# Performance work log

Hardware: AMD Instinct MI355X
Metric: run time of the kernel (lower is better)

## Reference

```python
import jax, jax.numpy as jnp
import numpy as np

EPS = 1e-5  # BatchNorm eps (torch default)


def setup_inputs() -> dict:
    key = jax.random.key(0)
    ks = jax.random.split(key, 12)
    C, Ci, B, H, W = 64, 32, 2, 96, 96  # plane, inter_plane=plane//2

    def n(k, shape, s=0.05):
        return jax.random.normal(k, shape, jnp.float32) * s

    return {
        "xA": jax.random.normal(ks[0], (B, C, H, W), jnp.float32),
        "xB": jax.random.normal(ks[1], (B, C, H, W), jnp.float32),
        "Wk": n(ks[2], (Ci, C)), "bk": n(ks[3], (Ci,)),
        "Wv": n(ks[4], (Ci, C)), "bv": n(ks[5], (Ci,)),
        "Wq": n(ks[6], (Ci, C)), "bq": n(ks[7], (Ci,)),
        "Wg": n(ks[8], (Ci, Ci)),  # conv_wg, 1x1 Conv1d, no bias
        "g1_gamma": jnp.ones((Ci,), jnp.float32), "g1_beta": jnp.zeros((Ci,), jnp.float32),
        "g1_mean": jnp.zeros((Ci,), jnp.float32), "g1_var": jnp.ones((Ci,), jnp.float32),
        "Wo": n(ks[9], (C, Ci)), "bo": n(ks[10], (C,)),
        "g2_gamma": jnp.ones((C,), jnp.float32), "g2_beta": jnp.zeros((C,), jnp.float32),
        "g2_mean": jnp.zeros((C,), jnp.float32), "g2_var": jnp.ones((C,), jnp.float32),
    }


def reference(xA, xB, Wk, bk, Wv, bv, Wq, bq, Wg,
              g1_gamma, g1_beta, g1_mean, g1_var,
              Wo, bo, g2_gamma, g2_beta, g2_mean, g2_var):
    B, C, H, W = xB.shape
    N = H * W
    # 1x1 conv2d projections -> [B, Ci, N]
    k = (jnp.einsum('bchw,oc->bohw', xA, Wk) + bk[None, :, None, None]).reshape(B, -1, N)
    v = (jnp.einsum('bchw,oc->bohw', xA, Wv) + bv[None, :, None, None]).reshape(B, -1, N)
    q = (jnp.einsum('bchw,oc->bohw', xB, Wq) + bq[None, :, None, None]).reshape(B, -1, N)
    # AV = softmax(v^T @ q, axis=2)  -> [B, N, N]
    A = jax.nn.softmax(jnp.einsum('bcn,bcm->bnm', v, q), axis=2)
    # k @ AV -> [B, Ci, N]
    av = jnp.einsum('bcn,bnm->bcm', k, A)
    # conv_wg (1x1 conv1d, no bias) + BatchNorm1d (inference form)
    av = jnp.einsum('oc,bcn->bon', Wg, av)
    av = (av - g1_mean[None, :, None]) * (g1_gamma / jnp.sqrt(g1_var + EPS))[None, :, None] + g1_beta[None, :, None]
    av = av.reshape(B, -1, H, W)
    # out: 1x1 conv2d -> plane, BatchNorm2d, residual, relu
    o = jnp.einsum('oc,bchw->bohw', Wo, av) + bo[None, :, None, None]
    o = (o - g2_mean[None, :, None, None]) * (g2_gamma / jnp.sqrt(g2_var + EPS))[None, :, None, None] + g2_beta[None, :, None, None]
    return jax.nn.relu(o + xB)
```

## Files before the change

kernel.cpp:

```cpp
#include <hip/hip_runtime.h>
#include <hip/hip_bf16.h>

#define CI 32
#define CC 64
#define NBATCH 2
#define NPIX 9216
#define NSD 16
#define LOG2E 1.4426950408889634f

typedef __attribute__((ext_vector_type(8))) short s16x8;
typedef __attribute__((ext_vector_type(4))) short s16x4;
typedef __attribute__((ext_vector_type(4))) float f32x4;
typedef __attribute__((ext_vector_type(2))) unsigned int u32x2;
typedef __attribute__((ext_vector_type(4))) unsigned int u32x4;

static __device__ __forceinline__ unsigned cvtpk(float a, float b) {
    unsigned d;
    asm("v_cvt_pk_bf16_f32 %0, %1, %2" : "=v"(d) : "v"(a), "v"(b));
    return d;
}
static __device__ __forceinline__ short f2b(float f) {
    union { float f; unsigned u; } v; v.f = f;
    return (short)((v.u + 0x7FFFu + ((v.u >> 16) & 1u)) >> 16);
}
static __device__ __forceinline__ float b2f(short s) {
    union { unsigned u; float f; } v; v.u = ((unsigned)(unsigned short)s) << 16;
    return v.f;
}

__global__ __launch_bounds__(256) void k_proj(
    const float* __restrict__ xA, const float* __restrict__ xB,
    const float* __restrict__ Wk, const float* __restrict__ bk,
    const float* __restrict__ Wv, const float* __restrict__ bv,
    const float* __restrict__ Wq, const float* __restrict__ bq,
    short* __restrict__ vT, short* __restrict__ qT, short* __restrict__ kC)
{
    int mode = blockIdx.y;
    const float* W    = mode == 0 ? Wk : (mode == 1 ? Wv : Wq);
    const float* bias = mode == 0 ? bk : (mode == 1 ? bv : bq);
    const float* X    = mode == 2 ? xB : xA;

    __shared__ float sW[CI * CC];
    __shared__ float sb[CI];
    __shared__ float spart[3][64][33];
    for (int i = threadIdx.x; i < CI * CC; i += 256) sW[i] = W[i];
    if (threadIdx.x < CI) sb[threadIdx.x] = bias[threadIdx.x];
    __syncthreads();

    int q4 = threadIdx.x >> 6;
    int lp = threadIdx.x & 63;
    int idx = blockIdx.x * 64 + lp;
    int b = idx / NPIX, n = idx % NPIX;

    float acc[CI];
    #pragma unroll
    for (int o = 0; o < CI; o++) acc[o] = 0.f;

    const float* px = X + (size_t)b * CC * NPIX + n;
    #pragma unroll
    for (int cc = 0; cc < 16; cc++) {
        int c = q4 * 16 + cc;
        float x = px[(size_t)c * NPIX];
        #pragma unroll
        for (int o = 0; o < CI; o++) acc[o] += sW[o * CC + c] * x;
    }
    if (q4) {
        #pragma unroll
        for (int o = 0; o < CI; o++) spart[q4 - 1][lp][o] = acc[o];
    }
    __syncthreads();
    if (q4 == 0) {
        #pragma unroll
        for (int o = 0; o < CI; o++)
            acc[o] += spart[0][lp][o] + spart[1][lp][o] + spart[2][lp][o] + sb[o];
        if (mode == 0) {
            #pragma unroll
            for (int o = 0; o < CI; o++)
                kC[((size_t)b * CI + o) * NPIX + n] = f2b(acc[o]);
        } else {
            float sc = (mode == 2) ? LOG2E : 1.0f;
            short* dst = (mode == 1 ? vT : qT) + ((size_t)b * NPIX + n) * CI;
            #pragma unroll
            for (int v4 = 0; v4 < 4; v4++) {
                u32x4 pk;
                #pragma unroll
                for (int j = 0; j < 4; j++)
                    pk[j] = cvtpk(acc[v4 * 8 + 2 * j] * sc, acc[v4 * 8 + 2 * j + 1] * sc);
                ((u32x4*)dst)[v4] = pk;
            }
        }
    }
}

__global__ __launch_bounds__(128) void k_denom(
    const short* __restrict__ vT, const short* __restrict__ qT,
    float* __restrict__ sum_part)
{
    int w = threadIdx.x >> 6, lane = threadIdx.x & 63;
    int r = lane & 15, g = lane >> 4;
    int b = blockIdx.y;
    int nb = blockIdx.x * 64 + w * 32;

    const short* vb = vT + (size_t)b * NPIX * CI;
    s16x8 a0 = *(const s16x8*)(vb + (size_t)(nb + r) * CI + 8 * g);
    s16x8 a1 = *(const s16x8*)(vb + (size_t)(nb + 16 + r) * CI + 8 * g);

    f32x4 s0 = {0.f, 0.f, 0.f, 0.f}, s1 = {0.f, 0.f, 0.f, 0.f};
    f32x4 z  = {0.f, 0.f, 0.f, 0.f};
    const short* qb = qT + (size_t)b * NPIX * CI;
    int mlo = blockIdx.z * (NPIX / NSD);
    int mhi = mlo + NPIX / NSD;
    for (int m0 = mlo; m0 < mhi; m0 += 32) {
        s16x8 q0 = *(const s16x8*)(qb + (size_t)(m0 + r) * CI + 8 * g);
        s16x8 q1 = *(const s16x8*)(qb + (size_t)(m0 + 16 + r) * CI + 8 * g);
        f32x4 t00 = __builtin_amdgcn_mfma_f32_16x16x32_bf16(a0, q0, z, 0, 0, 0);
        f32x4 t01 = __builtin_amdgcn_mfma_f32_16x16x32_bf16(a0, q1, z, 0, 0, 0);
        f32x4 t10 = __builtin_amdgcn_mfma_f32_16x16x32_bf16(a1, q0, z, 0, 0, 0);
        f32x4 t11 = __builtin_amdgcn_mfma_f32_16x16x32_bf16(a1, q1, z, 0, 0, 0);
        #pragma unroll
        for (int e = 0; e < 4; e++) {
            s0[e] += __builtin_amdgcn_exp2f(t00[e]) + __builtin_amdgcn_exp2f(t01[e]);
            s1[e] += __builtin_amdgcn_exp2f(t10[e]) + __builtin_amdgcn_exp2f(t11[e]);
        }
    }
    #pragma unroll
    for (int mask = 1; mask < 16; mask <<= 1) {
        #pragma unroll
        for (int e = 0; e < 4; e++) {
            s0[e] += __shfl_xor(s0[e], mask, 64);
            s1[e] += __shfl_xor(s1[e], mask, 64);
        }
    }
    if (r == 0) {
        float* sp = sum_part + ((size_t)blockIdx.z * NBATCH + b) * NPIX;
        #pragma unroll
        for (int e = 0; e < 4; e++) {
            sp[nb + 4 * g + e]      = s0[e];
            sp[nb + 16 + 4 * g + e] = s1[e];
        }
    }
}

__global__ __launch_bounds__(256) void k_invd(
    const float* __restrict__ sum_part, float* __restrict__ invd)
{
    int idx = blockIdx.x * 256 + threadIdx.x;
    float s = 0.f;
    #pragma unroll
    for (int zz = 0; zz < NSD; zz++)
        s += sum_part[(size_t)zz * NBATCH * NPIX + idx];
    invd[idx] = 1.0f / s;
}

__global__ __launch_bounds__(256) void k_scale(
    short* __restrict__ kC, const float* __restrict__ invd)
{
    int idx = blockIdx.x * 256 + threadIdx.x;
    int n = idx % NPIX;
    int b = idx / (CI * NPIX);
    kC[idx] = f2b(b2f(kC[idx]) * invd[b * NPIX + n]);
}

__global__ __launch_bounds__(128) void k_attn(
    const short* __restrict__ vT, const short* __restrict__ qT,
    const short* __restrict__ kC, short* __restrict__ avp, int slice)
{
    __shared__ short plds[2][32][36];
    int w = threadIdx.x >> 6, lane = threadIdx.x & 63;
    int r = lane & 15, g = lane >> 4;
    int b = blockIdx.y;
    int m0 = blockIdx.x * 64 + w * 32;

    const short* qb = qT + (size_t)b * NPIX * CI;
    s16x8 qb0 = *(const s16x8*)(qb + (size_t)(m0 + r) * CI + 8 * g);
    s16x8 qb1 = *(const s16x8*)(qb + (size_t)(m0 + 16 + r) * CI + 8 * g);

    const short* vb = vT + (size_t)b * NPIX * CI;
    const short* k0 = kC + ((size_t)b * CI + r) * NPIX;
    const short* k1 = k0 + (size_t)16 * NPIX;

    f32x4 acc00 = {0,0,0,0}, acc01 = {0,0,0,0}, acc10 = {0,0,0,0}, acc11 = {0,0,0,0};
    f32x4 z = {0,0,0,0};

    int nlo = blockIdx.z * slice;
    int nhi = nlo + slice;
    for (int n0 = nlo; n0 < nhi; n0 += 32) {
        s16x8 a0  = *(const s16x8*)(vb + (size_t)(n0 + r) * CI + 8 * g);
        s16x8 a1  = *(const s16x8*)(vb + (size_t)(n0 + 16 + r) * CI + 8 * g);
        s16x8 ka0 = *(const s16x8*)(k0 + n0 + 8 * g);
        s16x8 ka1 = *(const s16x8*)(k1 + n0 + 8 * g);

        f32x4 t00 = __builtin_amdgcn_mfma_f32_16x16x32_bf16(a0, qb0, z, 0, 0, 0);
        f32x4 t01 = __builtin_amdgcn_mfma_f32_16x16x32_bf16(a0, qb1, z, 0, 0, 0);
        f32x4 t10 = __builtin_amdgcn_mfma_f32_16x16x32_bf16(a1, qb0, z, 0, 0, 0);
        f32x4 t11 = __builtin_amdgcn_mfma_f32_16x16x32_bf16(a1, qb1, z, 0, 0, 0);

        u32x2 w00 = {cvtpk(__builtin_amdgcn_exp2f(t00[0]), __builtin_amdgcn_exp2f(t00[1])),
                     cvtpk(__builtin_amdgcn_exp2f(t00[2]), __builtin_amdgcn_exp2f(t00[3]))};
        u32x2 w10 = {cvtpk(__builtin_amdgcn_exp2f(t10[0]), __builtin_amdgcn_exp2f(t10[1])),
                     cvtpk(__builtin_amdgcn_exp2f(t10[2]), __builtin_amdgcn_exp2f(t10[3]))};
        u32x2 w01 = {cvtpk(__builtin_amdgcn_exp2f(t01[0]), __builtin_amdgcn_exp2f(t01[1])),
                     cvtpk(__builtin_amdgcn_exp2f(t01[2]), __builtin_amdgcn_exp2f(t01[3]))};
        u32x2 w11 = {cvtpk(__builtin_amdgcn_exp2f(t11[0]), __builtin_amdgcn_exp2f(t11[1])),
                     cvtpk(__builtin_amdgcn_exp2f(t11[2]), __builtin_amdgcn_exp2f(t11[3]))};

        *(u32x2*)&plds[w][r][4 * g]           = w00;
        *(u32x2*)&plds[w][r][16 + 4 * g]      = w10;
        *(u32x2*)&plds[w][16 + r][4 * g]      = w01;
        *(u32x2*)&plds[w][16 + r][16 + 4 * g] = w11;

        s16x4 l0 = *(const s16x4*)&plds[w][r][8 * g];
        s16x4 h0 = *(const s16x4*)&plds[w][r][8 * g + 4];
        s16x4 l1 = *(const s16x4*)&plds[w][16 + r][8 * g];
        s16x4 h1 = *(const s16x4*)&plds[w][16 + r][8 * g + 4];
        s16x8 pb0 = {l0[0], l0[1], l0[2], l0[3], h0[0], h0[1], h0[2], h0[3]};
        s16x8 pb1 = {l1[0], l1[1], l1[2], l1[3], h1[0], h1[1], h1[2], h1[3]};

        acc00 = __builtin_amdgcn_mfma_f32_16x16x32_bf16(ka0, pb0, acc00, 0, 0, 0);
        acc10 = __builtin_amdgcn_mfma_f32_16x16x32_bf16(ka1, pb0, acc10, 0, 0, 0);
        acc01 = __builtin_amdgcn_mfma_f32_16x16x32_bf16(ka0, pb1, acc01, 0, 0, 0);
        acc11 = __builtin_amdgcn_mfma_f32_16x16x32_bf16(ka1, pb1, acc11, 0, 0, 0);
    }

    short* dst = avp + ((size_t)blockIdx.z * NBATCH + b) * NPIX * CI;
    u32x2 o00 = {cvtpk(acc00[0], acc00[1]), cvtpk(acc00[2], acc00[3])};
    u32x2 o10 = {cvtpk(acc10[0], acc10[1]), cvtpk(acc10[2], acc10[3])};
    u32x2 o01 = {cvtpk(acc01[0], acc01[1]), cvtpk(acc01[2], acc01[3])};
    u32x2 o11 = {cvtpk(acc11[0], acc11[1]), cvtpk(acc11[2], acc11[3])};
    *(u32x2*)(dst + (size_t)(m0 + r) * CI + 4 * g)           = o00;
    *(u32x2*)(dst + (size_t)(m0 + r) * CI + 16 + 4 * g)      = o10;
    *(u32x2*)(dst + (size_t)(m0 + 16 + r) * CI + 4 * g)      = o01;
    *(u32x2*)(dst + (size_t)(m0 + 16 + r) * CI + 16 + 4 * g) = o11;
}

__global__ __launch_bounds__(256) void e_red(
    const short* __restrict__ avp, short* __restrict__ av, int nsa)
{
    int vecidx = blockIdx.x * 256 + threadIdx.x;
    const short* src = avp + (size_t)vecidx * 8;
    float s[8];
    #pragma unroll
    for (int j = 0; j < 8; j++) s[j] = 0.f;
    for (int zz = 0; zz < nsa; zz++) {
        s16x8 t = *(const s16x8*)(src + (size_t)zz * NBATCH * NPIX * CI);
        #pragma unroll
        for (int j = 0; j < 8; j++) s[j] += b2f(t[j]);
    }
    u32x4 pk;
    #pragma unroll
    for (int j = 0; j < 4; j++) pk[j] = cvtpk(s[2 * j], s[2 * j + 1]);
    *(u32x4*)(av + (size_t)vecidx * 8) = pk;
}

__global__ __launch_bounds__(256) void e_fused(
    const short* __restrict__ av,
    const float* __restrict__ Wg,
    const float* __restrict__ g1g, const float* __restrict__ g1b,
    const float* __restrict__ g1m, const float* __restrict__ g1v,
    const float* __restrict__ Wo, const float* __restrict__ bo,
    const float* __restrict__ g2g, const float* __restrict__ g2b,
    const float* __restrict__ g2m, const float* __restrict__ g2v,
    const float* __restrict__ xB, float* __restrict__ out)
{
    __shared__ float sWg[CI * CI], sWo[32 * CI], s1[CI], t1[CI], s2[32], t2[32];
    int t = threadIdx.x, jh = blockIdx.y;
    for (int i = t; i < CI * CI; i += 256) sWg[i] = Wg[i];
    for (int i = t; i < 32 * CI; i += 256) sWo[i] = Wo[jh * 32 * CI + i];
    if (t < CI) {
        float s = g1g[t] * rsqrtf(g1v[t] + 1e-5f);
        s1[t] = s; t1[t] = g1b[t] - g1m[t] * s;
    } else if (t < CI + 32) {
        int j = jh * 32 + (t - CI);
        float s = g2g[j] * rsqrtf(g2v[j] + 1e-5f);
        s2[t - CI] = s; t2[t - CI] = g2b[j] - g2m[j] * s + bo[j] * s;
    }
    __syncthreads();

    int idx = blockIdx.x * 256 + t;
    int b = idx / NPIX, m = idx % NPIX;

    float a[CI];
    const short* p = av + (size_t)idx * CI;
    #pragma unroll
    for (int v8 = 0; v8 < 4; v8++) {
        s16x8 tv = *(const s16x8*)(p + 8 * v8);
        #pragma unroll
        for (int j = 0; j < 8; j++) a[8 * v8 + j] = b2f(tv[j]);
    }
    float a2[CI];
    #pragma unroll
    for (int o = 0; o < CI; o++) {
        float acc = 0.f;
        #pragma unroll
        for (int c = 0; c < CI; c++) acc += sWg[o * CI + c] * a[c];
        a2[o] = acc * s1[o] + t1[o];
    }
    #pragma unroll
    for (int jj = 0; jj < 32; jj++) {
        float acc = 0.f;
        #pragma unroll
        for (int o = 0; o < CI; o++) acc += sWo[jj * CI + o] * a2[o];
        acc = acc * s2[jj] + t2[jj];
        size_t oi = ((size_t)b * CC + jh * 32 + jj) * NPIX + m;
        float res = acc + xB[oi];
        out[oi] = res > 0.f ? res : 0.f;
    }
}

extern "C" void kernel_launch(void* const* d_in, const int* in_sizes, int n_in,
                              void* d_out, int out_size, void* d_ws, size_t ws_size,
                              hipStream_t stream)
{
    const float* xA = (const float*)d_in[0];
    const float* xB = (const float*)d_in[1];
    const float* Wk = (const float*)d_in[2];
    const float* bk = (const float*)d_in[3];
    const float* Wv = (const float*)d_in[4];
    const float* bv = (const float*)d_in[5];
    const float* Wq = (const float*)d_in[6];
    const float* bq = (const float*)d_in[7];
    const float* Wg = (const float*)d_in[8];
    const float* g1g = (const float*)d_in[9];
    const float* g1b = (const float*)d_in[10];
    const float* g1m = (const float*)d_in[11];
    const float* g1v = (const float*)d_in[12];
    const float* Wo = (const float*)d_in[13];
    const float* bo = (const float*)d_in[14];
    const float* g2g = (const float*)d_in[15];
    const float* g2b = (const float*)d_in[16];
    const float* g2m = (const float*)d_in[17];
    const float* g2v = (const float*)d_in[18];
    float* out = (float*)d_out;

    char* ws = (char*)d_ws;
    const size_t SZB = (size_t)NBATCH * NPIX * CI * 2;
    short* vT = (short*)(ws);
    short* qT = (short*)(ws + SZB);
    short* kC = (short*)(ws + 2 * SZB);
    float* invd = (float*)(ws + 3 * SZB);
    char*  region = ws + 3 * SZB + (size_t)NBATCH * NPIX * 4;
    float* sum_part = (float*)region;
    short* avp = (short*)region;
    short* av = vT;

    const size_t base = 3 * SZB + (size_t)NBATCH * NPIX * 4;
    int nsa = (ws_size >= base + (size_t)16 * NBATCH * NPIX * CI * 2) ? 16 : 8;
    int slice = NPIX / nsa;

    k_proj<<<dim3(NBATCH * NPIX / 64, 3), dim3(256), 0, stream>>>(
        xA, xB, Wk, bk, Wv, bv, Wq, bq, vT, qT, kC);
    k_denom<<<dim3(NPIX / 64, NBATCH, NSD), dim3(128), 0, stream>>>(
        vT, qT, sum_part);
    k_invd<<<dim3(NBATCH * NPIX / 256), dim3(256), 0, stream>>>(
        sum_part, invd);
    k_scale<<<dim3(NBATCH * CI * NPIX / 256), dim3(256), 0, stream>>>(
        kC, invd);
    k_attn<<<dim3(NPIX / 64, NBATCH, nsa), dim3(128), 0, stream>>>(
        vT, qT, kC, avp, slice);
    e_red<<<dim3(NBATCH * NPIX * CI / 8 / 256), dim3(256), 0, stream>>>(
        avp, av, nsa);
    e_fused<<<dim3(NBATCH * NPIX / 256, 2), dim3(256), 0, stream>>>(
        av, Wg, g1g, g1b, g1m, g1v, Wo, bo, g2g, g2b, g2m, g2v, xB, out);
}
```

Baseline: 140.2 us.

## Retune denominator split, unroll attention loops, and widen reduction and epilogue grids

The denominator pass is split across more key slices (24 instead of 16), and its inner loop now handles 64 keys per iteration with a second pair of accumulators. The attention loop processes two 32-key chunks per iteration, each with its own LDS staging buffer, to give the scheduler more independent work. The partial-sum reduction now has each thread handle one packed pair of bf16 values instead of eight, using narrower loads over more threads. The fused epilogue is split four ways over output channels instead of two, which adds parallelism but recomputes the Wg projection in twice as many blocks.

New measurement: 133.5 us. 1.05x faster.

```diff
diff --git a/kernel.cpp b/kernel.cpp
--- a/kernel.cpp
+++ b/kernel.cpp
@@ -5,7 +5,7 @@
 #define CC 64
 #define NBATCH 2
 #define NPIX 9216
-#define NSD 16
+#define NSD 24
 #define LOG2E 1.4426950408889634f
 
 typedef __attribute__((ext_vector_type(8))) short s16x8;
@@ -106,23 +106,34 @@
     s16x8 a1 = *(const s16x8*)(vb + (size_t)(nb + 16 + r) * CI + 8 * g);
 
     f32x4 s0 = {0.f, 0.f, 0.f, 0.f}, s1 = {0.f, 0.f, 0.f, 0.f};
+    f32x4 s0b = {0.f, 0.f, 0.f, 0.f}, s1b = {0.f, 0.f, 0.f, 0.f};
     f32x4 z  = {0.f, 0.f, 0.f, 0.f};
     const short* qb = qT + (size_t)b * NPIX * CI;
     int mlo = blockIdx.z * (NPIX / NSD);
     int mhi = mlo + NPIX / NSD;
-    for (int m0 = mlo; m0 < mhi; m0 += 32) {
+    for (int m0 = mlo; m0 < mhi; m0 += 64) {
         s16x8 q0 = *(const s16x8*)(qb + (size_t)(m0 + r) * CI + 8 * g);
         s16x8 q1 = *(const s16x8*)(qb + (size_t)(m0 + 16 + r) * CI + 8 * g);
+        s16x8 q2 = *(const s16x8*)(qb + (size_t)(m0 + 32 + r) * CI + 8 * g);
+        s16x8 q3 = *(const s16x8*)(qb + (size_t)(m0 + 48 + r) * CI + 8 * g);
         f32x4 t00 = __builtin_amdgcn_mfma_f32_16x16x32_bf16(a0, q0, z, 0, 0, 0);
         f32x4 t01 = __builtin_amdgcn_mfma_f32_16x16x32_bf16(a0, q1, z, 0, 0, 0);
         f32x4 t10 = __builtin_amdgcn_mfma_f32_16x16x32_bf16(a1, q0, z, 0, 0, 0);
         f32x4 t11 = __builtin_amdgcn_mfma_f32_16x16x32_bf16(a1, q1, z, 0, 0, 0);
+        f32x4 u00 = __builtin_amdgcn_mfma_f32_16x16x32_bf16(a0, q2, z, 0, 0, 0);
+        f32x4 u01 = __builtin_amdgcn_mfma_f32_16x16x32_bf16(a0, q3, z, 0, 0, 0);
+        f32x4 u10 = __builtin_amdgcn_mfma_f32_16x16x32_bf16(a1, q2, z, 0, 0, 0);
+        f32x4 u11 = __builtin_amdgcn_mfma_f32_16x16x32_bf16(a1, q3, z, 0, 0, 0);
         #pragma unroll
         for (int e = 0; e < 4; e++) {
-            s0[e] += __builtin_amdgcn_exp2f(t00[e]) + __builtin_amdgcn_exp2f(t01[e]);
-            s1[e] += __builtin_amdgcn_exp2f(t10[e]) + __builtin_amdgcn_exp2f(t11[e]);
-        }
-    }
+            s0[e]  += __builtin_amdgcn_exp2f(t00[e]) + __builtin_amdgcn_exp2f(t01[e]);
+            s1[e]  += __builtin_amdgcn_exp2f(t10[e]) + __builtin_amdgcn_exp2f(t11[e]);
+            s0b[e] += __builtin_amdgcn_exp2f(u00[e]) + __builtin_amdgcn_exp2f(u01[e]);
+            s1b[e] += __builtin_amdgcn_exp2f(u10[e]) + __builtin_amdgcn_exp2f(u11[e]);
+        }
+    }
+    #pragma unroll
+    for (int e = 0; e < 4; e++) { s0[e] += s0b[e]; s1[e] += s1b[e]; }
     #pragma unroll
     for (int mask = 1; mask < 16; mask <<= 1) {
         #pragma unroll
@@ -165,7 +176,7 @@
     const short* __restrict__ vT, const short* __restrict__ qT,
     const short* __restrict__ kC, short* __restrict__ avp, int slice)
 {
-    __shared__ short plds[2][32][36];
+    __shared__ short plds[2][2][32][36];
     int w = threadIdx.x >> 6, lane = threadIdx.x & 63;
     int r = lane & 15, g = lane >> 4;
     int b = blockIdx.y;
@@ -184,42 +195,46 @@
 
     int nlo = blockIdx.z * slice;
     int nhi = nlo + slice;
-    for (int n0 = nlo; n0 < nhi; n0 += 32) {
-        s16x8 a0  = *(const s16x8*)(vb + (size_t)(n0 + r) * CI + 8 * g);
-        s16x8 a1  = *(const s16x8*)(vb + (size_t)(n0 + 16 + r) * CI + 8 * g);
-        s16x8 ka0 = *(const s16x8*)(k0 + n0 + 8 * g);
-        s16x8 ka1 = *(const s16x8*)(k1 + n0 + 8 * g);
-
-        f32x4 t00 = __builtin_amdgcn_mfma_f32_16x16x32_bf16(a0, qb0, z, 0, 0, 0);
-        f32x4 t01 = __builtin_amdgcn_mfma_f32_16x16x32_bf16(a0, qb1, z, 0, 0, 0);
-        f32x4 t10 = __builtin_amdgcn_mfma_f32_16x16x32_bf16(a1, qb0, z, 0, 0, 0);
-        f32x4 t11 = __builtin_amdgcn_mfma_f32_16x16x32_bf16(a1, qb1, z, 0, 0, 0);
-
-        u32x2 w00 = {cvtpk(__builtin_amdgcn_exp2f(t00[0]), __builtin_amdgcn_exp2f(t00[1])),
-                     cvtpk(__builtin_amdgcn_exp2f(t00[2]), __builtin_amdgcn_exp2f(t00[3]))};
-        u32x2 w10 = {cvtpk(__builtin_amdgcn_exp2f(t10[0]), __builtin_amdgcn_exp2f(t10[1])),
-                     cvtpk(__builtin_amdgcn_exp2f(t10[2]), __builtin_amdgcn_exp2f(t10[3]))};
-        u32x2 w01 = {cvtpk(__builtin_amdgcn_exp2f(t01[0]), __builtin_amdgcn_exp2f(t01[1])),
-                     cvtpk(__builtin_amdgcn_exp2f(t01[2]), __builtin_amdgcn_exp2f(t01[3]))};
-        u32x2 w11 = {cvtpk(__builtin_amdgcn_exp2f(t11[0]), __builtin_amdgcn_exp2f(t11[1])),
-                     cvtpk(__builtin_amdgcn_exp2f(t11[2]), __builtin_amdgcn_exp2f(t11[3]))};
-
-        *(u32x2*)&plds[w][r][4 * g]           = w00;
-        *(u32x2*)&plds[w][r][16 + 4 * g]      = w10;
-        *(u32x2*)&plds[w][16 + r][4 * g]      = w01;
-        *(u32x2*)&plds[w][16 + r][16 + 4 * g] = w11;
-
-        s16x4 l0 = *(const s16x4*)&plds[w][r][8 * g];
-        s16x4 h0 = *(const s16x4*)&plds[w][r][8 * g + 4];
-        s16x4 l1 = *(const s16x4*)&plds[w][16 + r][8 * g];
-        s16x4 h1 = *(const s16x4*)&plds[w][16 + r][8 * g + 4];
-        s16x8 pb0 = {l0[0], l0[1], l0[2], l0[3], h0[0], h0[1], h0[2], h0[3]};
-        s16x8 pb1 = {l1[0], l1[1], l1[2], l1[3], h1[0], h1[1], h1[2], h1[3]};
-
-        acc00 = __builtin_amdgcn_mfma_f32_16x16x32_bf16(ka0, pb0, acc00, 0, 0, 0);
-        acc10 = __builtin_amdgcn_mfma_f32_16x16x32_bf16(ka1, pb0, acc10, 0, 0, 0);
-        acc01 = __builtin_amdgcn_mfma_f32_16x16x32_bf16(ka0, pb1, acc01, 0, 0, 0);
-        acc11 = __builtin_amdgcn_mfma_f32_16x16x32_bf16(ka1, pb1, acc11, 0, 0, 0);
+    for (int n0 = nlo; n0 < nhi; n0 += 64) {
+        #pragma unroll
+        for (int par = 0; par < 2; par++) {
+            int nn = n0 + par * 32;
+            s16x8 a0  = *(const s16x8*)(vb + (size_t)(nn + r) * CI + 8 * g);
+            s16x8 a1  = *(const s16x8*)(vb + (size_t)(nn + 16 + r) * CI + 8 * g);
+            s16x8 ka0 = *(const s16x8*)(k0 + nn + 8 * g);
+            s16x8 ka1 = *(const s16x8*)(k1 + nn + 8 * g);
+
+            f32x4 t00 = __builtin_amdgcn_mfma_f32_16x16x32_bf16(a0, qb0, z, 0, 0, 0);
+            f32x4 t01 = __builtin_amdgcn_mfma_f32_16x16x32_bf16(a0, qb1, z, 0, 0, 0);
+            f32x4 t10 = __builtin_amdgcn_mfma_f32_16x16x32_bf16(a1, qb0, z, 0, 0, 0);
+            f32x4 t11 = __builtin_amdgcn_mfma_f32_16x16x32_bf16(a1, qb1, z, 0, 0, 0);
+
+            u32x2 w00 = {cvtpk(__builtin_amdgcn_exp2f(t00[0]), __builtin_amdgcn_exp2f(t00[1])),
+                         cvtpk(__builtin_amdgcn_exp2f(t00[2]), __builtin_amdgcn_exp2f(t00[3]))};
+            u32x2 w10 = {cvtpk(__builtin_amdgcn_exp2f(t10[0]), __builtin_amdgcn_exp2f(t10[1])),
+                         cvtpk(__builtin_amdgcn_exp2f(t10[2]), __builtin_amdgcn_exp2f(t10[3]))};
+            u32x2 w01 = {cvtpk(__builtin_amdgcn_exp2f(t01[0]), __builtin_amdgcn_exp2f(t01[1])),
+                         cvtpk(__builtin_amdgcn_exp2f(t01[2]), __builtin_amdgcn_exp2f(t01[3]))};
+            u32x2 w11 = {cvtpk(__builtin_amdgcn_exp2f(t11[0]), __builtin_amdgcn_exp2f(t11[1])),
+                         cvtpk(__builtin_amdgcn_exp2f(t11[2]), __builtin_amdgcn_exp2f(t11[3]))};
+
+            *(u32x2*)&plds[w][par][r][4 * g]           = w00;
+            *(u32x2*)&plds[w][par][r][16 + 4 * g]      = w10;
+            *(u32x2*)&plds[w][par][16 + r][4 * g]      = w01;
+            *(u32x2*)&plds[w][par][16 + r][16 + 4 * g] = w11;
+
+            s16x4 l0 = *(const s16x4*)&plds[w][par][r][8 * g];
+            s16x4 h0 = *(const s16x4*)&plds[w][par][r][8 * g + 4];
+            s16x4 l1 = *(const s16x4*)&plds[w][par][16 + r][8 * g];
+            s16x4 h1 = *(const s16x4*)&plds[w][par][16 + r][8 * g + 4];
+            s16x8 pb0 = {l0[0], l0[1], l0[2], l0[3], h0[0], h0[1], h0[2], h0[3]};
+            s16x8 pb1 = {l1[0], l1[1], l1[2], l1[3], h1[0], h1[1], h1[2], h1[3]};
+
+            acc00 = __builtin_amdgcn_mfma_f32_16x16x32_bf16(ka0, pb0, acc00, 0, 0, 0);
+            acc10 = __builtin_amdgcn_mfma_f32_16x16x32_bf16(ka1, pb0, acc10, 0, 0, 0);
+            acc01 = __builtin_amdgcn_mfma_f32_16x16x32_bf16(ka0, pb1, acc01, 0, 0, 0);
+            acc11 = __builtin_amdgcn_mfma_f32_16x16x32_bf16(ka1, pb1, acc11, 0, 0, 0);
+        }
     }
 
     short* dst = avp + ((size_t)blockIdx.z * NBATCH + b) * NPIX * CI;
@@ -236,20 +251,15 @@
 __global__ __launch_bounds__(256) void e_red(
     const short* __restrict__ avp, short* __restrict__ av, int nsa)
 {
-    int vecidx = blockIdx.x * 256 + threadIdx.x;
-    const short* src = avp + (size_t)vecidx * 8;
-    float s[8];
-    #pragma unroll
-    for (int j = 0; j < 8; j++) s[j] = 0.f;
+    int idx = blockIdx.x * 256 + threadIdx.x;
+    const unsigned* src = (const unsigned*)avp;
+    float lo = 0.f, hi = 0.f;
     for (int zz = 0; zz < nsa; zz++) {
-        s16x8 t = *(const s16x8*)(src + (size_t)zz * NBATCH * NPIX * CI);
-        #pragma unroll
-        for (int j = 0; j < 8; j++) s[j] += b2f(t[j]);
-    }
-    u32x4 pk;
-    #pragma unroll
-    for (int j = 0; j < 4; j++) pk[j] = cvtpk(s[2 * j], s[2 * j + 1]);
-    *(u32x4*)(av + (size_t)vecidx * 8) = pk;
+        unsigned p = src[(size_t)zz * (NBATCH * NPIX * CI / 2) + idx];
+        lo += b2f((short)(p & 0xFFFF));
+        hi += b2f((short)(p >> 16));
+    }
+    ((unsigned*)av)[idx] = cvtpk(lo, hi);
 }
 
 __global__ __launch_bounds__(256) void e_fused(
@@ -262,15 +272,15 @@
     const float* __restrict__ g2m, const float* __restrict__ g2v,
     const float* __restrict__ xB, float* __restrict__ out)
 {
-    __shared__ float sWg[CI * CI], sWo[32 * CI], s1[CI], t1[CI], s2[32], t2[32];
-    int t = threadIdx.x, jh = blockIdx.y;
+    __shared__ float sWg[CI * CI], sWo[16 * CI], s1[CI], t1[CI], s2[16], t2[16];
+    int t = threadIdx.x, jq = blockIdx.y;
     for (int i = t; i < CI * CI; i += 256) sWg[i] = Wg[i];
-    for (int i = t; i < 32 * CI; i += 256) sWo[i] = Wo[jh * 32 * CI + i];
+    for (int i = t; i < 16 * CI; i += 256) sWo[i] = Wo[jq * 16 * CI + i];
     if (t < CI) {
         float s = g1g[t] * rsqrtf(g1v[t] + 1e-5f);
         s1[t] = s; t1[t] = g1b[t] - g1m[t] * s;
-    } else if (t < CI + 32) {
-        int j = jh * 32 + (t - CI);
+    } else if (t < CI + 16) {
+        int j = jq * 16 + (t - CI);
         float s = g2g[j] * rsqrtf(g2v[j] + 1e-5f);
         s2[t - CI] = s; t2[t - CI] = g2b[j] - g2m[j] * s + bo[j] * s;
     }
@@ -296,12 +306,12 @@
         a2[o] = acc * s1[o] + t1[o];
     }
     #pragma unroll
-    for (int jj = 0; jj < 32; jj++) {
+    for (int jj = 0; jj < 16; jj++) {
         float acc = 0.f;
         #pragma unroll
         for (int o = 0; o < CI; o++) acc += sWo[jj * CI + o] * a2[o];
         acc = acc * s2[jj] + t2[jj];
-        size_t oi = ((size_t)b * CC + jh * 32 + jj) * NPIX + m;
+        size_t oi = ((size_t)b * CC + jq * 16 + jj) * NPIX + m;
         float res = acc + xB[oi];
         out[oi] = res > 0.f ? res : 0.f;
     }
@@ -357,8 +367,8 @@
         kC, invd);
     k_attn<<<dim3(NPIX / 64, NBATCH, nsa), dim3(128), 0, stream>>>(
         vT, qT, kC, avp, slice);
-    e_red<<<dim3(NBATCH * NPIX * CI / 8 / 256), dim3(256), 0, stream>>>(
+    e_red<<<dim3(NBATCH * NPIX * CI / 2 / 256), dim3(256), 0, stream>>>(
         avp, av, nsa);
-    e_fused<<<dim3(NBATCH * NPIX / 256, 2), dim3(256), 0, stream>>>(
+    e_fused<<<dim3(NBATCH * NPIX / 256, 4), dim3(256), 0, stream>>>(
         av, Wg, g1g, g1b, g1m, g1v, Wo, bo, g2g, g2b, g2m, g2v, xB, out);
 }
```
